# Performance work log

Measured on AMD Instinct MI355X. Metric: run time of the kernel, lower is better.

## Reference

```python
import jax, jax.numpy as jnp
import numpy as np

PLP_ORDER = 16
N_CHANNEL = 40
FFT_LENGTH = 512
SAMPLE_RATE = 16000
LIFTER = 22
COMP_FACTOR = 0.33
FLOOR = 1e-5
F_MIN = 0.0
F_MAX = SAMPLE_RATE / 2


def _hz_to_mel(hz):
    return 1127.0 * np.log1p(np.asarray(hz, dtype=np.float64) / 700.0)


def _mel_to_hz(mel):
    return 700.0 * np.expm1(np.asarray(mel, dtype=np.float64) / 1127.0)


def _build_constants():
    # SPTK-style mel filter bank (triangular in mel domain).
    mel_min = _hz_to_mel(F_MIN)
    mel_max = _hz_to_mel(F_MAX)
    lower_bin = max(1, int(F_MIN / SAMPLE_RATE * FFT_LENGTH + 1.5))
    upper_bin = min(FFT_LENGTH // 2, int(F_MAX / SAMPLE_RATE * FFT_LENGTH + 0.5))
    seed = np.arange(1, N_CHANNEL + 2)
    cf_mel = (mel_max - mel_min) / (N_CHANNEL + 1) * seed + mel_min  # (C+1,)
    bins = np.arange(lower_bin, upper_bin)
    mel = _hz_to_mel(SAMPLE_RATE * bins / FFT_LENGTH)
    ch = np.searchsorted(cf_mel, mel, side='left')  # first center freq >= mel
    diff = cf_mel - np.concatenate([[mel_min], cf_mel[:-1]])
    w = (cf_mel[ch] - mel) / diff[ch]
    H = np.zeros((len(bins), N_CHANNEL))
    rows = np.arange(len(bins))
    low = ch - 1
    m_lo = low >= 0
    H[rows[m_lo], low[m_lo]] += w[m_lo]
    m_hi = ch <= N_CHANNEL - 1
    H[rows[m_hi], ch[m_hi]] += 1.0 - w[m_hi]
    # Equal-loudness curve over the first C center frequencies (in Hz).
    cf_hz = _mel_to_hz(cf_mel)
    f2 = cf_hz[:N_CHANNEL] ** 2
    eql = (f2 / (f2 + 160000.0)) ** 2 * (f2 + 1440000.0) / (f2 + 9610000.0)
    # Liftering vector, v[0] = 2.
    m = np.arange(PLP_ORDER + 1)
    lift = 1.0 + LIFTER / 2.0 * np.sin(np.pi / LIFTER * m)
    lift[0] = 2.0
    return lower_bin, upper_bin, H.astype(np.float32), eql.astype(np.float32), lift.astype(np.float32)


LOWER_BIN, UPPER_BIN, H_NP, EQL_NP, LIFT_NP = _build_constants()


def _levinson_durbin(r):
    # r: (..., M+1) autocorrelation -> (gain K, LPC coefficients a_1..a_M)
    M = PLP_ORDER
    E = r[..., 0]
    a = jnp.zeros(r.shape[:-1] + (M,), r.dtype)
    for i in range(1, M + 1):
        acc = r[..., i]
        if i > 1:
            acc = acc + jnp.einsum('...j,...j->...', a[..., : i - 1], r[..., 1:i][..., ::-1])
        k = -acc / E
        if i > 1:
            a = a.at[..., : i - 1].set(a[..., : i - 1] + k[..., None] * a[..., : i - 1][..., ::-1])
        a = a.at[..., i - 1].set(k)
        E = E * (1.0 - k * k)
    return jnp.sqrt(E), a


def _lpc_to_cepstrum(K, a):
    # c0 = log K; c_m = -a_m - sum_{k=1}^{m-1} (k/m) c_k a_{m-k}
    M = PLP_ORDER
    c = [jnp.log(K)]
    for m in range(1, M + 1):
        acc = a[..., m - 1]
        for k in range(1, m):
            acc = acc + (k / m) * c[k] * a[..., m - k - 1]
        c.append(-acc)
    return jnp.stack(c, axis=-1)  # (..., M+1)


def _plp(x):
    H = jnp.asarray(H_NP)
    eql = jnp.asarray(EQL_NP)
    lift = jnp.asarray(LIFT_NP)
    # Mel filter bank on power spectrum (use_power=True)
    fb = jnp.matmul(x[..., LOWER_BIN:UPPER_BIN], H)          # (..., C)
    logfb = jnp.log(jnp.maximum(fb, FLOOR))
    # Equal-loudness scaling + cubic-root amplitude compression
    y = (jnp.exp(logfb) * eql) ** COMP_FACTOR                # (..., C)
    # replicate1: duplicate first and last channels
    y = jnp.concatenate([y[..., :1], y, y[..., -1:]], axis=-1)  # (..., C+2)
    n = y.shape[-1]
    # hfft with norm='forward' -> inverse-FFT-like autocorrelation
    r = jnp.fft.hfft(y) / (2 * (n - 1))
    r = r[..., : PLP_ORDER + 1]
    K, a = _levinson_durbin(r)
    c = _lpc_to_cepstrum(K, a)
    c = c * lift
    return c[..., 1:]  # out_format 'y': PLP without C0, (..., M)


def setup_inputs() -> dict:
    key = jax.random.key(0)
    x = jax.random.uniform(key, (32, 4096, FFT_LENGTH // 2 + 1), dtype=jnp.float32)
    return {"x": x}


def reference(x):
    return _plp(x)
```

## Files before the change

### kernel.cpp

```cpp
#include <hip/hip_runtime.h>

#define NCH   40
#define MORD  16
#define NR    17
#define NY    42
#define NBINS 257
#define FPB   64

namespace cfg {

constexpr double PI  = 3.14159265358979323846264338327950288;
constexpr double LN2 = 0.693147180559945309417232121458176568;

constexpr double cexp(double x) {
    double t = 1.0, s = 1.0;
    for (int i = 1; i < 40; ++i) { t *= x / i; s += t; }
    return s;
}

constexpr double clog(double z) {
    double lg = 0.0;
    while (z > 1.4142135623730951) { z *= 0.5; lg += LN2; }
    while (z < 0.7071067811865476) { z *= 2.0; lg -= LN2; }
    double u = (z - 1.0) / (z + 1.0), u2 = u * u, t = u, s = u;
    for (int k = 1; k < 24; ++k) { t *= u2; s += t / (2.0 * k + 1.0); }
    return lg + 2.0 * s;
}

constexpr double ccos(double x) {
    double tp = 2.0 * PI;
    double q = x / tp;
    long long k = (long long)(q + (q >= 0.0 ? 0.5 : -0.5));
    double r = x - (double)k * tp;
    double r2 = r * r, t = 1.0, s = 1.0;
    for (int i = 1; i < 20; ++i) { t *= -r2 / ((2.0 * i - 1.0) * (2.0 * i)); s += t; }
    return s;
}

constexpr double csin(double x) { return ccos(x - PI / 2.0); }

struct Tab {
    int   start[43];
    float w[257];
    float eql[NCH];
    float lift[NR];
    float ct[NR][NY];
    constexpr Tab() : start(), w(), eql(), lift(), ct() {
        const double lmax  = clog(87.0 / 7.0);
        const double U1127 = lmax / 41.0;
        for (int c = 0; c <= 41; ++c) {
            double thr = 22.4 * (cexp((double)c * U1127) - 1.0);
            int s = (int)thr + 1;
            if (s < 1) s = 1;
            if (s > 256) s = 256;
            start[c] = s;
        }
        start[42 - 1] = start[41];
        for (int c = 0; c <= 40; ++c) {
            for (int b = start[c]; b < start[c + 1]; ++b) {
                double mel = 1127.0 * clog(1.0 + (double)b * 31.25 / 700.0);
                double t   = mel / (1127.0 * U1127);
                w[b] = (float)(t - (double)c);
            }
        }
        for (int c = 0; c < NCH; ++c) {
            double cf = 700.0 * (cexp((double)(c + 1) * U1127) - 1.0);
            double f2 = cf * cf;
            double e  = f2 / (f2 + 160000.0);
            e = e * e * (f2 + 1440000.0) / (f2 + 9610000.0);
            eql[c] = (float)e;
        }
        for (int m = 0; m < NR; ++m)
            lift[m] = (float)(1.0 + 11.0 * csin(PI * (double)m / 22.0));
        lift[0] = 2.0f;
        for (int l = 0; l < NR; ++l)
            for (int j = 0; j < NY; ++j) {
                double s = (j == 0 || j == NY - 1) ? 1.0 : 2.0;
                ct[l][j] = (float)(s * ccos(PI * (double)(j * l) / 41.0) / 82.0);
            }
    }
};

constexpr Tab T{};

}

__global__ __launch_bounds__(FPB) void plp_kernel(const float* __restrict__ x,
                                                  float* __restrict__ out,
                                                  int nframes)
{
    using cfg::T;
    __shared__ float slab[FPB * NBINS];
    const int tid = threadIdx.x;
    const long long F0 = (long long)blockIdx.x * FPB;

    {
        const float* base = x + F0 * NBINS + tid * 4;
        const float* gend = x + (long long)nframes * NBINS;
        #pragma unroll
        for (int k = 0; k < 65; ++k) {
            const int off = (k < 64) ? k * 256 : (FPB * NBINS - 256);
            const float* src = base + off;
            if (src + 4 > gend) src = gend - 4;
            __builtin_amdgcn_global_load_lds(
                (const __attribute__((address_space(1))) void*)src,
                (__attribute__((address_space(3))) void*)(slab + off),
                16, 0, 0);
        }
    }
    __syncthreads();

    const long long frame = F0 + tid;
    if (frame >= nframes) return;
    const float* __restrict__ fr = slab + tid * NBINS;

    float fb[NCH];
    #pragma unroll
    for (int c = 0; c < NCH; ++c) fb[c] = 0.f;

    #pragma unroll
    for (int c = 0; c <= 40; ++c) {
        #pragma unroll
        for (int b = T.start[c]; b < T.start[c + 1]; ++b) {
            float xv = fr[b];
            const float wa = T.w[b];
            if (c < 40) fb[c]     = fmaf(wa, xv, fb[c]);
            if (c >= 1) fb[c - 1] = fmaf(1.0f - wa, xv, fb[c - 1]);
        }
    }

    float ys[NY];
    #pragma unroll
    for (int c = 0; c < NCH; ++c) {
        float v = fmaxf(fb[c], 1e-5f) * T.eql[c];
        ys[c + 1] = __expf(0.33f * __logf(v));
    }
    ys[0] = ys[1];
    ys[NY - 1] = ys[NY - 2];

    float r[NR];
    #pragma unroll
    for (int l = 0; l < NR; ++l) {
        float acc = 0.f;
        #pragma unroll
        for (int j = 0; j < NY; ++j) acc = fmaf(T.ct[l][j], ys[j], acc);
        r[l] = acc;
    }

    float a[MORD];
    #pragma unroll
    for (int i = 0; i < MORD; ++i) a[i] = 0.f;
    float E = r[0];
    #pragma unroll
    for (int i = 1; i <= MORD; ++i) {
        float acc = r[i];
        #pragma unroll
        for (int j = 0; j < i - 1; ++j) acc = fmaf(a[j], r[i - 1 - j], acc);
        float k = -acc / E;
        const int half = (i - 1) / 2;
        #pragma unroll
        for (int j = 0; j < half; ++j) {
            float t1 = a[j], t2 = a[i - 2 - j];
            a[j]         = fmaf(k, t2, t1);
            a[i - 2 - j] = fmaf(k, t1, t2);
        }
        if ((i - 1) & 1) a[half] = fmaf(k, a[half], a[half]);
        a[i - 1] = k;
        E = E * (1.f - k * k);
    }

    float cc[NR];
    #pragma unroll
    for (int m = 1; m <= MORD; ++m) {
        float acc = a[m - 1];
        #pragma unroll
        for (int k2 = 1; k2 < m; ++k2)
            acc = fmaf(((float)k2 / (float)m) * cc[k2], a[m - k2 - 1], acc);
        cc[m] = -acc;
    }

    float o[16];
    #pragma unroll
    for (int m = 1; m <= MORD; ++m) o[m - 1] = cc[m] * T.lift[m];

    float4* op = reinterpret_cast<float4*>(out + (size_t)frame * 16);
    op[0] = make_float4(o[0],  o[1],  o[2],  o[3]);
    op[1] = make_float4(o[4],  o[5],  o[6],  o[7]);
    op[2] = make_float4(o[8],  o[9],  o[10], o[11]);
    op[3] = make_float4(o[12], o[13], o[14], o[15]);
}

extern "C" void kernel_launch(void* const* d_in, const int* in_sizes, int n_in,
                              void* d_out, int out_size, void* d_ws, size_t ws_size,
                              hipStream_t stream) {
    const float* x   = (const float*)d_in[0];
    float*      outp = (float*)d_out;
    int nframes = in_sizes[0] / NBINS;
    int nblocks = (nframes + FPB - 1) / FPB;
    plp_kernel<<<nblocks, FPB, 0, stream>>>(x, outp, nframes);
}
```

Measured before the change: 204.6 us.

## Double-buffer LDS slabs across multiple frame tiles per block with async prefetch

Each block now handles eight 64-frame slabs in sequence. Two LDS buffers hold the slabs, and the global_load_lds of the next slab is issued before the current one is computed, with an explicit vmcnt wait instead of a barrier. The goal is to hide global-load latency behind the per-frame PLP compute, and a fast path drops the per-load bounds clamp. The division in Levinson-Durbin is replaced by a hardware reciprocal. The cost is double the LDS per block and a grid eight times smaller, so only about one wave runs per CU, which may leave SIMDs idle for this compute-heavy kernel.

```diff
diff --git a/kernel.cpp b/kernel.cpp
--- a/kernel.cpp
+++ b/kernel.cpp
@@ -1,11 +1,14 @@
 #include <hip/hip_runtime.h>
 
-#define NCH   40
-#define MORD  16
-#define NR    17
-#define NY    42
-#define NBINS 257
-#define FPB   64
+#define NCH    40
+#define MORD   16
+#define NR     17
+#define NY     42
+#define NBINS  257
+#define FPB    64
+#define SLABS  8
+#define SLABF  (FPB * NBINS)
+#define NLD    65
 
 namespace cfg {
 
@@ -85,109 +88,135 @@
 
 }
 
-__global__ __launch_bounds__(FPB) void plp_kernel(const float* __restrict__ x,
-                                                  float* __restrict__ out,
-                                                  int nframes)
+__global__ __launch_bounds__(FPB, 1) void plp_kernel(const float* __restrict__ x,
+                                                     float* __restrict__ out,
+                                                     int nframes)
 {
     using cfg::T;
-    __shared__ float slab[FPB * NBINS];
+    __shared__ float slab[2][SLABF];
     const int tid = threadIdx.x;
-    const long long F0 = (long long)blockIdx.x * FPB;
-
-    {
-        const float* base = x + F0 * NBINS + tid * 4;
-        const float* gend = x + (long long)nframes * NBINS;
-        #pragma unroll
-        for (int k = 0; k < 65; ++k) {
-            const int off = (k < 64) ? k * 256 : (FPB * NBINS - 256);
-            const float* src = base + off;
-            if (src + 4 > gend) src = gend - 4;
-            __builtin_amdgcn_global_load_lds(
-                (const __attribute__((address_space(1))) void*)src,
-                (__attribute__((address_space(3))) void*)(slab + off),
-                16, 0, 0);
+    const long long blk    = blockIdx.x;
+    const long long blkF0  = blk * (long long)(SLABS * FPB);
+    const float* gblk = x + blkF0 * NBINS;
+    const float* gend = x + (long long)nframes * NBINS;
+    const bool safe = (blkF0 + SLABS * FPB) <= (long long)nframes;
+
+    auto stage = [&](int buf, int s) {
+        const float* base = gblk + (long long)s * SLABF + tid * 4;
+        float* lbase = &slab[buf][0];
+        if (safe) {
+            #pragma unroll
+            for (int k = 0; k < NLD; ++k) {
+                const int off = (k < 64) ? k * 256 : (SLABF - 256);
+                __builtin_amdgcn_global_load_lds(
+                    (const __attribute__((address_space(1))) void*)(base + off),
+                    (__attribute__((address_space(3))) void*)(lbase + off),
+                    16, 0, 0);
+            }
+        } else {
+            #pragma unroll
+            for (int k = 0; k < NLD; ++k) {
+                const int off = (k < 64) ? k * 256 : (SLABF - 256);
+                const float* src = base + off;
+                if (src + 4 > gend) src = gend - 4;
+                __builtin_amdgcn_global_load_lds(
+                    (const __attribute__((address_space(1))) void*)src,
+                    (__attribute__((address_space(3))) void*)(lbase + off),
+                    16, 0, 0);
+            }
+        }
+    };
+
+    stage(0, 0);
+
+    #pragma unroll 1
+    for (int s = 0; s < SLABS; ++s) {
+        if (s + 1 < SLABS) {
+            stage((s + 1) & 1, s + 1);
+            asm volatile("s_waitcnt vmcnt(32)" ::: "memory");
+        } else {
+            asm volatile("s_waitcnt vmcnt(0)" ::: "memory");
+        }
+
+        const long long frame = blkF0 + (long long)s * FPB + tid;
+        if (frame < nframes) {
+            const float* fr = &slab[s & 1][tid * NBINS];
+
+            float fb[NCH];
+            #pragma unroll
+            for (int c = 0; c < NCH; ++c) fb[c] = 0.f;
+            #pragma unroll
+            for (int c = 0; c <= 40; ++c) {
+                #pragma unroll
+                for (int b = T.start[c]; b < T.start[c + 1]; ++b) {
+                    float xv = fr[b];
+                    const float wa = T.w[b];
+                    if (c < 40) fb[c]     = fmaf(wa, xv, fb[c]);
+                    if (c >= 1) fb[c - 1] = fmaf(1.0f - wa, xv, fb[c - 1]);
+                }
+            }
+
+            float ys[NY];
+            #pragma unroll
+            for (int c = 0; c < NCH; ++c) {
+                float v = fmaxf(fb[c], 1e-5f) * T.eql[c];
+                ys[c + 1] = __expf(0.33f * __logf(v));
+            }
+            ys[0] = ys[1];
+            ys[NY - 1] = ys[NY - 2];
+
+            float r[NR];
+            #pragma unroll
+            for (int l = 0; l < NR; ++l) {
+                float acc = 0.f;
+                #pragma unroll
+                for (int j = 0; j < NY; ++j) acc = fmaf(T.ct[l][j], ys[j], acc);
+                r[l] = acc;
+            }
+
+            float a[MORD];
+            #pragma unroll
+            for (int i = 0; i < MORD; ++i) a[i] = 0.f;
+            float E = r[0];
+            #pragma unroll
+            for (int i = 1; i <= MORD; ++i) {
+                float acc = r[i];
+                #pragma unroll
+                for (int j = 0; j < i - 1; ++j) acc = fmaf(a[j], r[i - 1 - j], acc);
+                float k = -acc * __builtin_amdgcn_rcpf(E);
+                const int half = (i - 1) / 2;
+                #pragma unroll
+                for (int j = 0; j < half; ++j) {
+                    float t1 = a[j], t2 = a[i - 2 - j];
+                    a[j]         = fmaf(k, t2, t1);
+                    a[i - 2 - j] = fmaf(k, t1, t2);
+                }
+                if ((i - 1) & 1) a[half] = fmaf(k, a[half], a[half]);
+                a[i - 1] = k;
+                E = E * (1.f - k * k);
+            }
+
+            float cc[NR];
+            #pragma unroll
+            for (int m = 1; m <= MORD; ++m) {
+                float acc = a[m - 1];
+                #pragma unroll
+                for (int k2 = 1; k2 < m; ++k2)
+                    acc = fmaf(((float)k2 / (float)m) * cc[k2], a[m - k2 - 1], acc);
+                cc[m] = -acc;
+            }
+
+            float o[16];
+            #pragma unroll
+            for (int m = 1; m <= MORD; ++m) o[m - 1] = cc[m] * T.lift[m];
+
+            float4* op = reinterpret_cast<float4*>(out + (size_t)frame * 16);
+            op[0] = make_float4(o[0],  o[1],  o[2],  o[3]);
+            op[1] = make_float4(o[4],  o[5],  o[6],  o[7]);
+            op[2] = make_float4(o[8],  o[9],  o[10], o[11]);
+            op[3] = make_float4(o[12], o[13], o[14], o[15]);
         }
     }
-    __syncthreads();
-
-    const long long frame = F0 + tid;
-    if (frame >= nframes) return;
-    const float* __restrict__ fr = slab + tid * NBINS;
-
-    float fb[NCH];
-    #pragma unroll
-    for (int c = 0; c < NCH; ++c) fb[c] = 0.f;
-
-    #pragma unroll
-    for (int c = 0; c <= 40; ++c) {
-        #pragma unroll
-        for (int b = T.start[c]; b < T.start[c + 1]; ++b) {
-            float xv = fr[b];
-            const float wa = T.w[b];
-            if (c < 40) fb[c]     = fmaf(wa, xv, fb[c]);
-            if (c >= 1) fb[c - 1] = fmaf(1.0f - wa, xv, fb[c - 1]);
-        }
-    }
-
-    float ys[NY];
-    #pragma unroll
-    for (int c = 0; c < NCH; ++c) {
-        float v = fmaxf(fb[c], 1e-5f) * T.eql[c];
-        ys[c + 1] = __expf(0.33f * __logf(v));
-    }
-    ys[0] = ys[1];
-    ys[NY - 1] = ys[NY - 2];
-
-    float r[NR];
-    #pragma unroll
-    for (int l = 0; l < NR; ++l) {
-        float acc = 0.f;
-        #pragma unroll
-        for (int j = 0; j < NY; ++j) acc = fmaf(T.ct[l][j], ys[j], acc);
-        r[l] = acc;
-    }
-
-    float a[MORD];
-    #pragma unroll
-    for (int i = 0; i < MORD; ++i) a[i] = 0.f;
-    float E = r[0];
-    #pragma unroll
-    for (int i = 1; i <= MORD; ++i) {
-        float acc = r[i];
-        #pragma unroll
-        for (int j = 0; j < i - 1; ++j) acc = fmaf(a[j], r[i - 1 - j], acc);
-        float k = -acc / E;
-        const int half = (i - 1) / 2;
-        #pragma unroll
-        for (int j = 0; j < half; ++j) {
-            float t1 = a[j], t2 = a[i - 2 - j];
-            a[j]         = fmaf(k, t2, t1);
-            a[i - 2 - j] = fmaf(k, t1, t2);
-        }
-        if ((i - 1) & 1) a[half] = fmaf(k, a[half], a[half]);
-        a[i - 1] = k;
-        E = E * (1.f - k * k);
-    }
-
-    float cc[NR];
-    #pragma unroll
-    for (int m = 1; m <= MORD; ++m) {
-        float acc = a[m - 1];
-        #pragma unroll
-        for (int k2 = 1; k2 < m; ++k2)
-            acc = fmaf(((float)k2 / (float)m) * cc[k2], a[m - k2 - 1], acc);
-        cc[m] = -acc;
-    }
-
-    float o[16];
-    #pragma unroll
-    for (int m = 1; m <= MORD; ++m) o[m - 1] = cc[m] * T.lift[m];
-
-    float4* op = reinterpret_cast<float4*>(out + (size_t)frame * 16);
-    op[0] = make_float4(o[0],  o[1],  o[2],  o[3]);
-    op[1] = make_float4(o[4],  o[5],  o[6],  o[7]);
-    op[2] = make_float4(o[8],  o[9],  o[10], o[11]);
-    op[3] = make_float4(o[12], o[13], o[14], o[15]);
 }
 
 extern "C" void kernel_launch(void* const* d_in, const int* in_sizes, int n_in,
@@ -196,6 +225,6 @@
     const float* x   = (const float*)d_in[0];
     float*      outp = (float*)d_out;
     int nframes = in_sizes[0] / NBINS;
-    int nblocks = (nframes + FPB - 1) / FPB;
+    int nblocks = (nframes + SLABS * FPB - 1) / (SLABS * FPB);
     plp_kernel<<<nblocks, FPB, 0, stream>>>(x, outp, nframes);
 }
```

Result: slower. 213.4 us (+4.3%).

## Stage spectra as fp16 in LDS, fold the cosine transform, double frames per block

Applied to the files above, without the earlier changes.

Replaces the async global-to-LDS float copy with per-thread float loads that are converted to half2 and stored in a padded fp16 shared slab. Only bins 1..256 are staged, and each block now covers 128 frames. The autocorrelation cosine transform is folded into even/odd symmetric sums, which halves its FMAs. The Levinson division becomes a hardware reciprocal and the cepstrum recursion precomputes the k/m scaling. Half-precision staging loses input precision and may affect accuracy, and the synchronous loads give up the direct-to-LDS path.

```diff
diff --git a/kernel.cpp b/kernel.cpp
--- a/kernel.cpp
+++ b/kernel.cpp
@@ -1,11 +1,12 @@
 #include <hip/hip_runtime.h>
+#include <hip/hip_fp16.h>
 
 #define NCH   40
 #define MORD  16
 #define NR    17
-#define NY    42
 #define NBINS 257
-#define FPB   64
+#define FPB   128
+#define FSTR  258
 
 namespace cfg {
 
@@ -41,11 +42,12 @@
 
 struct Tab {
     int   start[43];
+    int   chan[257];
     float w[257];
     float eql[NCH];
     float lift[NR];
-    float ct[NR][NY];
-    constexpr Tab() : start(), w(), eql(), lift(), ct() {
+    float ctf[NR][21];
+    constexpr Tab() : start(), chan(), w(), eql(), lift(), ctf() {
         const double lmax  = clog(87.0 / 7.0);
         const double U1127 = lmax / 41.0;
         for (int c = 0; c <= 41; ++c) {
@@ -55,12 +57,13 @@
             if (s > 256) s = 256;
             start[c] = s;
         }
-        start[42 - 1] = start[41];
+        start[42] = start[41];
         for (int c = 0; c <= 40; ++c) {
             for (int b = start[c]; b < start[c + 1]; ++b) {
                 double mel = 1127.0 * clog(1.0 + (double)b * 31.25 / 700.0);
                 double t   = mel / (1127.0 * U1127);
                 w[b] = (float)(t - (double)c);
+                chan[b] = c;
             }
         }
         for (int c = 0; c < NCH; ++c) {
@@ -74,9 +77,9 @@
             lift[m] = (float)(1.0 + 11.0 * csin(PI * (double)m / 22.0));
         lift[0] = 2.0f;
         for (int l = 0; l < NR; ++l)
-            for (int j = 0; j < NY; ++j) {
-                double s = (j == 0 || j == NY - 1) ? 1.0 : 2.0;
-                ct[l][j] = (float)(s * ccos(PI * (double)(j * l) / 41.0) / 82.0);
+            for (int j = 0; j <= 20; ++j) {
+                double s = (j == 0) ? 1.0 : 2.0;
+                ctf[l][j] = (float)(s * ccos(PI * (double)(j * l) / 41.0) / 82.0);
             }
     }
 };
@@ -90,60 +93,81 @@
                                                   int nframes)
 {
     using cfg::T;
-    __shared__ float slab[FPB * NBINS];
+    __shared__ __half slab[FPB * FSTR];
     const int tid = threadIdx.x;
     const long long F0 = (long long)blockIdx.x * FPB;
 
     {
-        const float* base = x + F0 * NBINS + tid * 4;
-        const float* gend = x + (long long)nframes * NBINS;
-        #pragma unroll
-        for (int k = 0; k < 65; ++k) {
-            const int off = (k < 64) ? k * 256 : (FPB * NBINS - 256);
-            const float* src = base + off;
-            if (src + 4 > gend) src = gend - 4;
-            __builtin_amdgcn_global_load_lds(
-                (const __attribute__((address_space(1))) void*)src,
-                (__attribute__((address_space(3))) void*)(slab + off),
-                16, 0, 0);
+        const int s  = tid >> 6;
+        const int ll = tid & 63;
+        __half2* l2 = reinterpret_cast<__half2*>(slab);
+        #pragma unroll 8
+        for (int r = 0; r < 64; ++r) {
+            const int fl = 2 * r + s;
+            long long fg = F0 + fl;
+            if (fg > (long long)nframes - 1) fg = (long long)nframes - 1;
+            const float* g = x + fg * NBINS + 1 + 4 * ll;
+            float x0 = g[0], x1 = g[1], x2 = g[2], x3 = g[3];
+            const int d = fl * 129 + 2 * ll;
+            l2[d]     = __float22half2_rn(make_float2(x0, x1));
+            l2[d + 1] = __float22half2_rn(make_float2(x2, x3));
         }
     }
     __syncthreads();
 
     const long long frame = F0 + tid;
     if (frame >= nframes) return;
-    const float* __restrict__ fr = slab + tid * NBINS;
+    const __half2* fr2 = reinterpret_cast<const __half2*>(slab) + tid * 129;
 
     float fb[NCH];
     #pragma unroll
     for (int c = 0; c < NCH; ++c) fb[c] = 0.f;
 
     #pragma unroll
-    for (int c = 0; c <= 40; ++c) {
-        #pragma unroll
-        for (int b = T.start[c]; b < T.start[c + 1]; ++b) {
-            float xv = fr[b];
-            const float wa = T.w[b];
-            if (c < 40) fb[c]     = fmaf(wa, xv, fb[c]);
-            if (c >= 1) fb[c - 1] = fmaf(1.0f - wa, xv, fb[c - 1]);
-        }
-    }
-
-    float ys[NY];
+    for (int p = 0; p < 128; ++p) {
+        float2 xp = __half22float2(fr2[p]);
+        {
+            constexpr int b = 1;
+            (void)b;
+        }
+        {
+            const int   bb = 2 * p + 1;
+            const int   c  = T.chan[bb];
+            const float wa = T.w[bb];
+            if (c < 40) fb[c]     = fmaf(wa, xp.x, fb[c]);
+            if (c >= 1) fb[c - 1] = fmaf(1.0f - wa, xp.x, fb[c - 1]);
+        }
+        if (2 * p + 2 <= 255) {
+            const int   bb = 2 * p + 2;
+            const int   c  = T.chan[bb];
+            const float wa = T.w[bb];
+            if (c < 40) fb[c]     = fmaf(wa, xp.y, fb[c]);
+            if (c >= 1) fb[c - 1] = fmaf(1.0f - wa, xp.y, fb[c - 1]);
+        }
+    }
+
+    float yv[NCH];
     #pragma unroll
     for (int c = 0; c < NCH; ++c) {
         float v = fmaxf(fb[c], 1e-5f) * T.eql[c];
-        ys[c + 1] = __expf(0.33f * __logf(v));
-    }
-    ys[0] = ys[1];
-    ys[NY - 1] = ys[NY - 2];
+        yv[c] = __expf(0.33f * __logf(v));
+    }
+
+    float ye[21], yo[21];
+    ye[0] = yv[0] + yv[39];  yo[0] = yv[0] - yv[39];
+    #pragma unroll
+    for (int j = 1; j <= 20; ++j) {
+        float aa = yv[j - 1], bb = yv[40 - j];
+        ye[j] = aa + bb;  yo[j] = aa - bb;
+    }
 
     float r[NR];
     #pragma unroll
     for (int l = 0; l < NR; ++l) {
+        const float* yy = (l & 1) ? yo : ye;
         float acc = 0.f;
         #pragma unroll
-        for (int j = 0; j < NY; ++j) acc = fmaf(T.ct[l][j], ys[j], acc);
+        for (int j = 0; j <= 20; ++j) acc = fmaf(T.ctf[l][j], yy[j], acc);
         r[l] = acc;
     }
 
@@ -156,7 +180,7 @@
         float acc = r[i];
         #pragma unroll
         for (int j = 0; j < i - 1; ++j) acc = fmaf(a[j], r[i - 1 - j], acc);
-        float k = -acc / E;
+        float k = -acc * __builtin_amdgcn_rcpf(E);
         const int half = (i - 1) / 2;
         #pragma unroll
         for (int j = 0; j < half; ++j) {
@@ -169,14 +193,16 @@
         E = E * (1.f - k * k);
     }
 
-    float cc[NR];
+    float cc[NR], ccs[NR];
     #pragma unroll
     for (int m = 1; m <= MORD; ++m) {
-        float acc = a[m - 1];
+        float acc = 0.f;
         #pragma unroll
         for (int k2 = 1; k2 < m; ++k2)
-            acc = fmaf(((float)k2 / (float)m) * cc[k2], a[m - k2 - 1], acc);
-        cc[m] = -acc;
+            acc = fmaf(ccs[k2], a[m - k2 - 1], acc);
+        float cm = -(a[m - 1] + acc * (1.0f / (float)m));
+        cc[m]  = cm;
+        ccs[m] = (float)m * cm;
     }
 
     float o[16];
```

After: 195.7 us. 4.3% less time.
